# Optimization experiments

Measured on AMD Instinct MI355X. Metric: run time of the kernel, lower is better.

Reference implementation:

```python
import jax, jax.numpy as jnp
import numpy as np

# Malvar-He-Cutler demosaic kernels: 4 output feature maps from the 1-channel bayer mosaic.
_K = [
    0, 0, -2, 0, 0,  0, 0, 4, 0, 0,  -2, 4, 8, 4, -2,  0, 0, 4, 0, 0,  0, 0, -2, 0, 0,
    0, 0, -3, 0, 0,  0, 4, 0, 4, 0,  -3, 0, 12, 0, -3,  0, 4, 0, 4, 0,  0, 0, -3, 0, 0,
    0, 0, 1, 0, 0,  0, -2, 0, -2, 0,  -2, 8, 10, 8, -2,  0, -2, 0, -2, 0,  0, 0, 1, 0, 0,
    0, 0, -2, 0, 0,  0, -2, 8, -2, 0,  1, 0, 10, 0, 1,  0, -2, 8, -2, 0,  0, 0, -2, 0, 0,
]
KERNELS = jnp.asarray(np.asarray(_K, dtype=np.float32).reshape(4, 1, 5, 5) / 16.0)
# Per-output-channel (R,G,B), per-quadrant (2x2) source channel into feats=(conv4 || x) -> 5 channels.
INDICES_RGGB = np.array([4, 2, 3, 1, 0, 4, 4, 0, 1, 3, 2, 4]).reshape(1, 3, 2, 2)


def _calc_index(pattern):
    p = tuple(np.asarray(pattern).flatten().tolist())
    if p == (0, 1, 1, 2):
        return INDICES_RGGB
    if p == (1, 0, 2, 1):
        return np.roll(INDICES_RGGB, 1, axis=-1)
    if p == (1, 2, 0, 1):
        return np.roll(INDICES_RGGB, 1, axis=-2)
    if p == (2, 1, 1, 0):
        return np.roll(np.roll(INDICES_RGGB, 1, axis=-1), 1, axis=-2)
    raise ValueError('Invalid bayer pattern')


def _pixel_shuffle(x, r):
    N, C, H, W = x.shape
    c = C // (r * r)
    return x.reshape(N, c, r, r, H, W).transpose(0, 1, 4, 2, 5, 3).reshape(N, c, H * r, W * r)


def _gather_bayer(x, index):
    """x: (N, C_in, H, W); index: (1|N, C_out, 2, 2) -> (N, C_out, H, W).
    Efficient equivalent of the original one-hot mask multiply-sum: a direct
    per-quadrant channel selection via take_along_axis."""
    N, C, H, W = x.shape
    iN, Cout = index.shape[0], index.shape[1]
    h, w = H // 2, W // 2
    # pixel_unshuffle(x,2) with channel order c*4 + (2*i + j): quadrant axis q.
    xq = x.reshape(N, C, h, 2, w, 2).transpose(0, 1, 3, 5, 2, 4).reshape(N, C, 4, h, w)
    xq = xq.swapaxes(1, 2)  # (N, 4, C, h, w)
    iq = index.reshape(iN, Cout, 4).swapaxes(1, 2)  # (iN, 4, Cout)
    iq = jnp.broadcast_to(iq, (N, 4, Cout))
    gath = jnp.take_along_axis(xq, iq[:, :, :, None, None], axis=2)  # (N, 4, Cout, h, w)
    y_down = gath.swapaxes(1, 2).reshape(N, Cout * 4, h, w)
    return _pixel_shuffle(y_down, 2)


def setup_inputs() -> dict:
    key = jax.random.key(0)
    x = jax.random.uniform(key, (16, 1, 1024, 1024), dtype=jnp.float32)
    bayer_pattern = jnp.array([0, 1, 1, 2], dtype=jnp.int64 if jax.config.jax_enable_x64 else jnp.int32).reshape(1, 1, 2, 2)  # RGGB
    return {"x": x, "bayer_pattern": bayer_pattern}


def reference(x, bayer_pattern) -> jnp.ndarray:
    # Replication pad by 2 on each side, then 5x5 conv producing 4 feature maps.
    x_pad = jnp.pad(x, ((0, 0), (0, 0), (2, 2), (2, 2)), mode='edge')
    feats = jax.lax.conv_general_dilated(
        x_pad, KERNELS.astype(x.dtype), window_strides=(1, 1), padding='VALID',
        dimension_numbers=('NCHW', 'OIHW', 'NCHW'))
    feats = jnp.concatenate([feats, x], axis=1)  # (N, 5, H, W)
    bp = np.asarray(bayer_pattern)  # bayer pattern is static metadata
    index = jnp.asarray(np.concatenate([_calc_index(bp[n]) for n in range(bp.shape[0])], axis=0))
    return _gather_bayer(feats, index)  # (N, 3, H, W)
```

## Files before the change

kernel.cpp:

```cpp
#include <hip/hip_runtime.h>


constexpr int H = 1024, W = 1024;
constexpr int TILE_W = 128, TILE_H = 32;
constexpr int LDS_W = TILE_W + 4;
constexpr int LDS_H = TILE_H + 4;
constexpr int CHUNKS_PER_ROW = LDS_W / 4;
constexpr int N_CHUNKS = CHUNKS_PER_ROW * LDS_H;

typedef float v4f __attribute__((ext_vector_type(4)));
typedef __attribute__((address_space(1))) const unsigned int gu32;
typedef __attribute__((address_space(3))) unsigned int lu32;

__global__ __launch_bounds__(256) void demosaic_kernel(
    const float* __restrict__ xin_all, const int* __restrict__ bp,
    float* __restrict__ out)
{
    __shared__ float tile[LDS_H][LDS_W];

    const int tx = threadIdx.x;
    const int ty = threadIdx.y;
    const int tid = ty * 32 + tx;
    const int x0 = blockIdx.x * TILE_W;
    const int y0 = blockIdx.y * TILE_H;
    const int n  = blockIdx.z;

    const int p0 = bp[0], p1 = bp[1];
    const int fi = (p0 == 2) || (p0 == 1 && p1 == 2);
    const int fj = (p0 == 2) || (p0 == 1 && p1 == 0);

    const float* __restrict__ xin = xin_all + (size_t)n * H * W;

    const int gx0 = x0 - 2;
    for (int idx = tid; idx < N_CHUNKS; idx += 256) {
        const int r = idx / CHUNKS_PER_ROW;
        const int k = idx - r * CHUNKS_PER_ROW;
        const int gy = min(max(y0 + r - 2, 0), H - 1);
        const int gx = min(max(gx0 + 4 * k, 0), W - 4);
        const float* src = xin + (size_t)gy * W + gx;
        __builtin_amdgcn_global_load_lds((gu32*)src, (lu32*)&tile[r][4 * k], 16, 0, 0);
    }
    __syncthreads();

    const bool left_edge  = (x0 == 0);
    const bool right_edge = (x0 == W - TILE_W);
    if (left_edge || right_edge) {
        if (tid < LDS_H) {
            const int r  = tid;
            const int gy = min(max(y0 + r - 2, 0), H - 1);
            const float* __restrict__ rowp = xin + (size_t)gy * W;
            if (left_edge) {
                tile[r][0] = rowp[0]; tile[r][1] = rowp[0];
                tile[r][2] = rowp[0]; tile[r][3] = rowp[1];
            }
            if (right_edge) {
                tile[r][128] = rowp[W - 2]; tile[r][129] = rowp[W - 1];
                tile[r][130] = rowp[W - 1]; tile[r][131] = rowp[W - 1];
            }
        }
        __syncthreads();
    }

    const int xs  = tx * 4;
    const int ry0 = ty * 4;

    float w[8][8];
    #pragma unroll
    for (int r = 0; r < 8; ++r) {
        const v4f a = *(const v4f*)&tile[ry0 + r][xs];
        const v4f b = *(const v4f*)&tile[ry0 + r][xs + 4];
        w[r][0] = a.x; w[r][1] = a.y; w[r][2] = a.z; w[r][3] = a.w;
        w[r][4] = b.x; w[r][5] = b.y; w[r][6] = b.z; w[r][7] = b.w;
    }

    #pragma unroll
    for (int dr = 0; dr < 4; ++dr) {
        const int qi = (dr & 1) ^ fi;

        float r4[4], g4[4], b4[4];
        #pragma unroll
        for (int p = 0; p < 4; ++p) {
            const float c   = w[dr + 2][p + 2];
            const float up  = w[dr + 1][p + 2], dn  = w[dr + 3][p + 2];
            const float lf  = w[dr + 2][p + 1], rt  = w[dr + 2][p + 3];
            const float up2 = w[dr + 0][p + 2], dn2 = w[dr + 4][p + 2];
            const float lf2 = w[dr + 2][p + 0], rt2 = w[dr + 2][p + 4];
            const float dg  = w[dr + 1][p + 1] + w[dr + 1][p + 3]
                            + w[dr + 3][p + 1] + w[dr + 3][p + 3];

            const float axH = lf2 + rt2;
            const float axV = up2 + dn2;
            const float ax  = axH + axV;
            const float crossHV = (up + dn) + (lf + rt);

            const float s0 = (8.0f  * c + 4.0f * crossHV   - 2.0f * ax) * 0.0625f;
            const float s1 = (12.0f * c + 4.0f * dg        - 3.0f * ax) * 0.0625f;
            const float s2 = (10.0f * c + 8.0f * (lf + rt) - 2.0f * (axH + dg) + axV) * 0.0625f;
            const float s3 = (10.0f * c + 8.0f * (up + dn) - 2.0f * (axV + dg) + axH) * 0.0625f;

            const int qj = (p & 1) ^ fj;
            const int qt = (qi << 1) | qj;
            r4[p] = (qt == 0) ? c  : (qt == 1) ? s2 : (qt == 2) ? s3 : s1;
            g4[p] = (qi == qj) ? s0 : c;
            b4[p] = (qt == 0) ? s1 : (qt == 1) ? s3 : (qt == 2) ? s2 : c;
        }

        const int y = y0 + ry0 + dr;
        const size_t colbase = (size_t)(x0 + xs);
        v4f* __restrict__ oR = (v4f*)(out + ((size_t)(n * 3 + 0) * H + y) * W + colbase);
        v4f* __restrict__ oG = (v4f*)(out + ((size_t)(n * 3 + 1) * H + y) * W + colbase);
        v4f* __restrict__ oB = (v4f*)(out + ((size_t)(n * 3 + 2) * H + y) * W + colbase);
        v4f vR = { r4[0], r4[1], r4[2], r4[3] };
        v4f vG = { g4[0], g4[1], g4[2], g4[3] };
        v4f vB = { b4[0], b4[1], b4[2], b4[3] };
        __builtin_nontemporal_store(vR, oR);
        __builtin_nontemporal_store(vG, oG);
        __builtin_nontemporal_store(vB, oB);
    }
}

extern "C" void kernel_launch(void* const* d_in, const int* in_sizes, int n_in,
                              void* d_out, int out_size, void* d_ws, size_t ws_size,
                              hipStream_t stream) {
    const float* x  = (const float*)d_in[0];
    const int*   bp = (const int*)d_in[1];
    float* out = (float*)d_out;
    const int N = in_sizes[0] / (H * W);
    dim3 grid(W / TILE_W, H / TILE_H, N);
    dim3 block(32, 8, 1);
    demosaic_kernel<<<grid, block, 0, stream>>>(x, bp, out);
}
```

Baseline: 244.3 us.

## Double-buffer LDS tiles across four row-tiles per block with async prefetch

Each block now processes four vertical tiles, using two LDS buffers. The global→LDS load of the next tile is issued before the current tile is computed, with manual vmcnt waits and barriers. Edge replication moves from a separate LDS fixup pass into register fixups inside a new rolling 5-row register window, and launch bounds request higher occupancy. The goal is to hide load latency and cut per-block overhead. The risks are the hand-counted vmcnt values, since the stores also count toward vmcnt, and a smaller grid.

```diff
diff --git a/kernel.cpp b/kernel.cpp
--- a/kernel.cpp
+++ b/kernel.cpp
@@ -3,6 +3,7 @@
 
 constexpr int H = 1024, W = 1024;
 constexpr int TILE_W = 128, TILE_H = 32;
+constexpr int NT = 4;
 constexpr int LDS_W = TILE_W + 4;
 constexpr int LDS_H = TILE_H + 4;
 constexpr int CHUNKS_PER_ROW = LDS_W / 4;
@@ -12,17 +13,17 @@
 typedef __attribute__((address_space(1))) const unsigned int gu32;
 typedef __attribute__((address_space(3))) unsigned int lu32;
 
-__global__ __launch_bounds__(256) void demosaic_kernel(
+__global__ __launch_bounds__(256, 4) void demosaic_kernel(
     const float* __restrict__ xin_all, const int* __restrict__ bp,
     float* __restrict__ out)
 {
-    __shared__ float tile[LDS_H][LDS_W];
+    __shared__ float tile[2][LDS_H][LDS_W];
 
     const int tx = threadIdx.x;
     const int ty = threadIdx.y;
     const int tid = ty * 32 + tx;
     const int x0 = blockIdx.x * TILE_W;
-    const int y0 = blockIdx.y * TILE_H;
+    const int ybase = blockIdx.y * (TILE_H * NT);
     const int n  = blockIdx.z;
 
     const int p0 = bp[0], p1 = bp[1];
@@ -30,93 +31,125 @@
     const int fj = (p0 == 2) || (p0 == 1 && p1 == 0);
 
     const float* __restrict__ xin = xin_all + (size_t)n * H * W;
+    const int gx0 = x0 - 2;
 
-    const int gx0 = x0 - 2;
-    for (int idx = tid; idx < N_CHUNKS; idx += 256) {
-        const int r = idx / CHUNKS_PER_ROW;
-        const int k = idx - r * CHUNKS_PER_ROW;
-        const int gy = min(max(y0 + r - 2, 0), H - 1);
-        const int gx = min(max(gx0 + 4 * k, 0), W - 4);
-        const float* src = xin + (size_t)gy * W + gx;
-        __builtin_amdgcn_global_load_lds((gu32*)src, (lu32*)&tile[r][4 * k], 16, 0, 0);
+    int rr[5]  = {0, 0, 0, 0, 0};
+    int gxo[5] = {0, 0, 0, 0, 0};
+    #pragma unroll
+    for (int j = 0; j < 5; ++j) {
+        const int idx = tid + 256 * j;
+        if (idx < N_CHUNKS) {
+            const int r = idx / CHUNKS_PER_ROW;
+            const int k = idx - r * CHUNKS_PER_ROW;
+            rr[j]  = r;
+            gxo[j] = min(max(gx0 + 4 * k, 0), W - 4);
+        }
     }
-    __syncthreads();
 
-    const bool left_edge  = (x0 == 0);
-    const bool right_edge = (x0 == W - TILE_W);
-    if (left_edge || right_edge) {
-        if (tid < LDS_H) {
-            const int r  = tid;
-            const int gy = min(max(y0 + r - 2, 0), H - 1);
-            const float* __restrict__ rowp = xin + (size_t)gy * W;
-            if (left_edge) {
-                tile[r][0] = rowp[0]; tile[r][1] = rowp[0];
-                tile[r][2] = rowp[0]; tile[r][3] = rowp[1];
-            }
-            if (right_edge) {
-                tile[r][128] = rowp[W - 2]; tile[r][129] = rowp[W - 1];
-                tile[r][130] = rowp[W - 1]; tile[r][131] = rowp[W - 1];
+    auto STAGE = [&](int buf, int y0) {
+        float* const base = &tile[buf][0][0];
+        #pragma unroll
+        for (int j = 0; j < 5; ++j) {
+            const int idx = tid + 256 * j;
+            if (idx < N_CHUNKS) {
+                const int gy = min(max(y0 + rr[j] - 2, 0), H - 1);
+                __builtin_amdgcn_global_load_lds(
+                    (gu32*)(xin + (size_t)gy * W + gxo[j]),
+                    (lu32*)(base + 4 * idx), 16, 0, 0);
             }
         }
-        __syncthreads();
-    }
+    };
+
+    const bool lfix = (x0 == 0) && (tx == 0);
+    const bool rfix = (x0 == W - TILE_W) && (tx == 31);
 
     const int xs  = tx * 4;
     const int ry0 = ty * 4;
 
-    float w[8][8];
-    #pragma unroll
-    for (int r = 0; r < 8; ++r) {
-        const v4f a = *(const v4f*)&tile[ry0 + r][xs];
-        const v4f b = *(const v4f*)&tile[ry0 + r][xs + 4];
-        w[r][0] = a.x; w[r][1] = a.y; w[r][2] = a.z; w[r][3] = a.w;
-        w[r][4] = b.x; w[r][5] = b.y; w[r][6] = b.z; w[r][7] = b.w;
-    }
+    auto LOAD_ROW = [&](float (&d)[8], const float* p) {
+        const v4f a = *(const v4f*)p;
+        const v4f b = *(const v4f*)(p + 4);
+        d[0] = a.x; d[1] = a.y; d[2] = a.z; d[3] = a.w;
+        d[4] = b.x; d[5] = b.y; d[6] = b.z; d[7] = b.w;
+        if (lfix) { d[3] = d[1]; d[1] = d[0]; d[2] = d[0]; }
+        if (rfix) { d[4] = d[6]; d[5] = d[7]; d[6] = d[7]; }
+    };
 
-    #pragma unroll
-    for (int dr = 0; dr < 4; ++dr) {
-        const int qi = (dr & 1) ^ fi;
+    auto COMPUTE = [&](int buf, int y0) {
+        float w[5][8];
+        #pragma unroll
+        for (int m = 0; m < 4; ++m) LOAD_ROW(w[m], &tile[buf][ry0 + m][xs]);
 
-        float r4[4], g4[4], b4[4];
         #pragma unroll
-        for (int p = 0; p < 4; ++p) {
-            const float c   = w[dr + 2][p + 2];
-            const float up  = w[dr + 1][p + 2], dn  = w[dr + 3][p + 2];
-            const float lf  = w[dr + 2][p + 1], rt  = w[dr + 2][p + 3];
-            const float up2 = w[dr + 0][p + 2], dn2 = w[dr + 4][p + 2];
-            const float lf2 = w[dr + 2][p + 0], rt2 = w[dr + 2][p + 4];
-            const float dg  = w[dr + 1][p + 1] + w[dr + 1][p + 3]
-                            + w[dr + 3][p + 1] + w[dr + 3][p + 3];
+        for (int dr = 0; dr < 4; ++dr) {
+            LOAD_ROW(w[(dr + 4) % 5], &tile[buf][ry0 + dr + 4][xs]);
+            #define WR_(m) (w[(dr + (m)) % 5])
+            const int qi = (dr & 1) ^ fi;
 
-            const float axH = lf2 + rt2;
-            const float axV = up2 + dn2;
-            const float ax  = axH + axV;
-            const float crossHV = (up + dn) + (lf + rt);
+            float r4[4], g4[4], b4[4];
+            #pragma unroll
+            for (int p = 0; p < 4; ++p) {
+                const float c   = WR_(2)[p + 2];
+                const float up  = WR_(1)[p + 2], dn  = WR_(3)[p + 2];
+                const float lf  = WR_(2)[p + 1], rt  = WR_(2)[p + 3];
+                const float up2 = WR_(0)[p + 2], dn2 = WR_(4)[p + 2];
+                const float lf2 = WR_(2)[p + 0], rt2 = WR_(2)[p + 4];
+                const float dg  = WR_(1)[p + 1] + WR_(1)[p + 3]
+                                + WR_(3)[p + 1] + WR_(3)[p + 3];
 
-            const float s0 = (8.0f  * c + 4.0f * crossHV   - 2.0f * ax) * 0.0625f;
-            const float s1 = (12.0f * c + 4.0f * dg        - 3.0f * ax) * 0.0625f;
-            const float s2 = (10.0f * c + 8.0f * (lf + rt) - 2.0f * (axH + dg) + axV) * 0.0625f;
-            const float s3 = (10.0f * c + 8.0f * (up + dn) - 2.0f * (axV + dg) + axH) * 0.0625f;
+                const float axH = lf2 + rt2;
+                const float axV = up2 + dn2;
+                const float ax  = axH + axV;
+                const float crossHV = (up + dn) + (lf + rt);
 
-            const int qj = (p & 1) ^ fj;
-            const int qt = (qi << 1) | qj;
-            r4[p] = (qt == 0) ? c  : (qt == 1) ? s2 : (qt == 2) ? s3 : s1;
-            g4[p] = (qi == qj) ? s0 : c;
-            b4[p] = (qt == 0) ? s1 : (qt == 1) ? s3 : (qt == 2) ? s2 : c;
+                const float s0 = (8.0f  * c + 4.0f * crossHV   - 2.0f * ax) * 0.0625f;
+                const float s1 = (12.0f * c + 4.0f * dg        - 3.0f * ax) * 0.0625f;
+                const float s2 = (10.0f * c + 8.0f * (lf + rt) - 2.0f * (axH + dg) + axV) * 0.0625f;
+                const float s3 = (10.0f * c + 8.0f * (up + dn) - 2.0f * (axV + dg) + axH) * 0.0625f;
+
+                const int qj = (p & 1) ^ fj;
+                const int qt = (qi << 1) | qj;
+                r4[p] = (qt == 0) ? c  : (qt == 1) ? s2 : (qt == 2) ? s3 : s1;
+                g4[p] = (qi == qj) ? s0 : c;
+                b4[p] = (qt == 0) ? s1 : (qt == 1) ? s3 : (qt == 2) ? s2 : c;
+            }
+            #undef WR_
+
+            const int y = y0 + ry0 + dr;
+            const size_t colbase = (size_t)(x0 + xs);
+            v4f* const oR = (v4f*)(out + ((size_t)(n * 3 + 0) * H + y) * W + colbase);
+            v4f* const oG = (v4f*)(out + ((size_t)(n * 3 + 1) * H + y) * W + colbase);
+            v4f* const oB = (v4f*)(out + ((size_t)(n * 3 + 2) * H + y) * W + colbase);
+            v4f vR = { r4[0], r4[1], r4[2], r4[3] };
+            v4f vG = { g4[0], g4[1], g4[2], g4[3] };
+            v4f vB = { b4[0], b4[1], b4[2], b4[3] };
+            __builtin_nontemporal_store(vR, oR);
+            __builtin_nontemporal_store(vG, oG);
+            __builtin_nontemporal_store(vB, oB);
         }
+    };
 
-        const int y = y0 + ry0 + dr;
-        const size_t colbase = (size_t)(x0 + xs);
-        v4f* __restrict__ oR = (v4f*)(out + ((size_t)(n * 3 + 0) * H + y) * W + colbase);
-        v4f* __restrict__ oG = (v4f*)(out + ((size_t)(n * 3 + 1) * H + y) * W + colbase);
-        v4f* __restrict__ oB = (v4f*)(out + ((size_t)(n * 3 + 2) * H + y) * W + colbase);
-        v4f vR = { r4[0], r4[1], r4[2], r4[3] };
-        v4f vG = { g4[0], g4[1], g4[2], g4[3] };
-        v4f vB = { b4[0], b4[1], b4[2], b4[3] };
-        __builtin_nontemporal_store(vR, oR);
-        __builtin_nontemporal_store(vG, oG);
-        __builtin_nontemporal_store(vB, oB);
-    }
+    STAGE(0, ybase + 0 * TILE_H);
+    STAGE(1, ybase + 1 * TILE_H);
+    asm volatile("s_waitcnt vmcnt(4)" ::: "memory");
+    __builtin_amdgcn_s_barrier();
+    COMPUTE(0, ybase + 0 * TILE_H);
+    __builtin_amdgcn_s_barrier();
+
+    STAGE(0, ybase + 2 * TILE_H);
+    asm volatile("s_waitcnt vmcnt(16)" ::: "memory");
+    __builtin_amdgcn_s_barrier();
+    COMPUTE(1, ybase + 1 * TILE_H);
+    __builtin_amdgcn_s_barrier();
+
+    STAGE(1, ybase + 3 * TILE_H);
+    asm volatile("s_waitcnt vmcnt(16)" ::: "memory");
+    __builtin_amdgcn_s_barrier();
+    COMPUTE(0, ybase + 2 * TILE_H);
+
+    asm volatile("s_waitcnt vmcnt(12)" ::: "memory");
+    __builtin_amdgcn_s_barrier();
+    COMPUTE(1, ybase + 3 * TILE_H);
 }
 
 extern "C" void kernel_launch(void* const* d_in, const int* in_sizes, int n_in,
@@ -126,7 +159,7 @@
     const int*   bp = (const int*)d_in[1];
     float* out = (float*)d_out;
     const int N = in_sizes[0] / (H * W);
-    dim3 grid(W / TILE_W, H / TILE_H, N);
+    dim3 grid(W / TILE_W, H / (TILE_H * NT), N);
     dim3 block(32, 8, 1);
     demosaic_kernel<<<grid, block, 0, stream>>>(x, bp, out);
 }
```

After: 258.1 us. 1.06x slower.

## Replace LDS tiling with register sliding window over rows per thread

Applied to the files above, without the earlier changes.

Drops the shared-memory tile and barrier and has each thread walk 16 output rows. It keeps a 5-row rolling register window filled by direct vectorized global loads of the left, center and right 4-float chunks, and prefetches the next row while the current one is computed. Halo reuse now relies on L1/L2 rather than LDS, so each thread reloads neighbours' chunks three times per row. Block shape and tile size also change, and launch bounds ask for 4 blocks per CU.

```diff
diff --git a/kernel.cpp b/kernel.cpp
--- a/kernel.cpp
+++ b/kernel.cpp
@@ -2,28 +2,21 @@
 
 
 constexpr int H = 1024, W = 1024;
-constexpr int TILE_W = 128, TILE_H = 32;
-constexpr int LDS_W = TILE_W + 4;
-constexpr int LDS_H = TILE_H + 4;
-constexpr int CHUNKS_PER_ROW = LDS_W / 4;
-constexpr int N_CHUNKS = CHUNKS_PER_ROW * LDS_H;
+constexpr int TILE_W = 256, TILE_H = 64;
+constexpr int RPT = 16;
 
 typedef float v4f __attribute__((ext_vector_type(4)));
-typedef __attribute__((address_space(1))) const unsigned int gu32;
-typedef __attribute__((address_space(3))) unsigned int lu32;
 
-__global__ __launch_bounds__(256) void demosaic_kernel(
+__global__ __launch_bounds__(256, 4) void demosaic_kernel(
     const float* __restrict__ xin_all, const int* __restrict__ bp,
     float* __restrict__ out)
 {
-    __shared__ float tile[LDS_H][LDS_W];
-
     const int tx = threadIdx.x;
     const int ty = threadIdx.y;
-    const int tid = ty * 32 + tx;
     const int x0 = blockIdx.x * TILE_W;
-    const int y0 = blockIdx.y * TILE_H;
     const int n  = blockIdx.z;
+    const int gx = x0 + tx * 4;
+    const int ry0 = blockIdx.y * TILE_H + ty * RPT;
 
     const int p0 = bp[0], p1 = bp[1];
     const int fi = (p0 == 2) || (p0 == 1 && p1 == 2);
@@ -31,62 +24,54 @@
 
     const float* __restrict__ xin = xin_all + (size_t)n * H * W;
 
-    const int gx0 = x0 - 2;
-    for (int idx = tid; idx < N_CHUNKS; idx += 256) {
-        const int r = idx / CHUNKS_PER_ROW;
-        const int k = idx - r * CHUNKS_PER_ROW;
-        const int gy = min(max(y0 + r - 2, 0), H - 1);
-        const int gx = min(max(gx0 + 4 * k, 0), W - 4);
-        const float* src = xin + (size_t)gy * W + gx;
-        __builtin_amdgcn_global_load_lds((gu32*)src, (lu32*)&tile[r][4 * k], 16, 0, 0);
-    }
-    __syncthreads();
+    const bool lfix = (gx == 0);
+    const bool rfix = (gx == W - 4);
+    const int xl = lfix ? 0  : gx - 4;
+    const int xr = rfix ? gx : gx + 4;
 
-    const bool left_edge  = (x0 == 0);
-    const bool right_edge = (x0 == W - TILE_W);
-    if (left_edge || right_edge) {
-        if (tid < LDS_H) {
-            const int r  = tid;
-            const int gy = min(max(y0 + r - 2, 0), H - 1);
-            const float* __restrict__ rowp = xin + (size_t)gy * W;
-            if (left_edge) {
-                tile[r][0] = rowp[0]; tile[r][1] = rowp[0];
-                tile[r][2] = rowp[0]; tile[r][3] = rowp[1];
-            }
-            if (right_edge) {
-                tile[r][128] = rowp[W - 2]; tile[r][129] = rowp[W - 1];
-                tile[r][130] = rowp[W - 1]; tile[r][131] = rowp[W - 1];
-            }
-        }
-        __syncthreads();
-    }
+    float w[5][8];
 
-    const int xs  = tx * 4;
-    const int ry0 = ty * 4;
+    auto LOADROW = [&](int gy, v4f& L, v4f& M, v4f& R) {
+        gy = min(max(gy, 0), H - 1);
+        const float* row = xin + (size_t)gy * W;
+        L = *(const v4f*)(row + xl);
+        M = *(const v4f*)(row + gx);
+        R = *(const v4f*)(row + xr);
+    };
+    auto INSERT = [&](float (&d)[8], v4f L, v4f M, v4f R) {
+        d[0] = lfix ? M.x : L.z;
+        d[1] = lfix ? M.x : L.w;
+        d[2] = M.x; d[3] = M.y; d[4] = M.z; d[5] = M.w;
+        d[6] = rfix ? M.w : R.x;
+        d[7] = rfix ? M.w : R.y;
+    };
 
-    float w[8][8];
-    #pragma unroll
-    for (int r = 0; r < 8; ++r) {
-        const v4f a = *(const v4f*)&tile[ry0 + r][xs];
-        const v4f b = *(const v4f*)&tile[ry0 + r][xs + 4];
-        w[r][0] = a.x; w[r][1] = a.y; w[r][2] = a.z; w[r][3] = a.w;
-        w[r][4] = b.x; w[r][5] = b.y; w[r][6] = b.z; w[r][7] = b.w;
+    {
+        v4f L[5], M[5], R[5];
+        #pragma unroll
+        for (int m = 0; m < 5; ++m) LOADROW(ry0 - 2 + m, L[m], M[m], R[m]);
+        #pragma unroll
+        for (int m = 0; m < 5; ++m) INSERT(w[m], L[m], M[m], R[m]);
     }
 
     #pragma unroll
-    for (int dr = 0; dr < 4; ++dr) {
+    for (int dr = 0; dr < RPT; ++dr) {
+        v4f Lp, Mp, Rp;
+        if (dr < RPT - 1) LOADROW(ry0 + dr + 3, Lp, Mp, Rp);
+
+        #define WR_(m) (w[(dr + (m)) % 5])
         const int qi = (dr & 1) ^ fi;
 
         float r4[4], g4[4], b4[4];
         #pragma unroll
         for (int p = 0; p < 4; ++p) {
-            const float c   = w[dr + 2][p + 2];
-            const float up  = w[dr + 1][p + 2], dn  = w[dr + 3][p + 2];
-            const float lf  = w[dr + 2][p + 1], rt  = w[dr + 2][p + 3];
-            const float up2 = w[dr + 0][p + 2], dn2 = w[dr + 4][p + 2];
-            const float lf2 = w[dr + 2][p + 0], rt2 = w[dr + 2][p + 4];
-            const float dg  = w[dr + 1][p + 1] + w[dr + 1][p + 3]
-                            + w[dr + 3][p + 1] + w[dr + 3][p + 3];
+            const float c   = WR_(2)[p + 2];
+            const float up  = WR_(1)[p + 2], dn  = WR_(3)[p + 2];
+            const float lf  = WR_(2)[p + 1], rt  = WR_(2)[p + 3];
+            const float up2 = WR_(0)[p + 2], dn2 = WR_(4)[p + 2];
+            const float lf2 = WR_(2)[p + 0], rt2 = WR_(2)[p + 4];
+            const float dg  = WR_(1)[p + 1] + WR_(1)[p + 3]
+                            + WR_(3)[p + 1] + WR_(3)[p + 3];
 
             const float axH = lf2 + rt2;
             const float axV = up2 + dn2;
@@ -104,18 +89,21 @@
             g4[p] = (qi == qj) ? s0 : c;
             b4[p] = (qt == 0) ? s1 : (qt == 1) ? s3 : (qt == 2) ? s2 : c;
         }
+        #undef WR_
 
-        const int y = y0 + ry0 + dr;
-        const size_t colbase = (size_t)(x0 + xs);
-        v4f* __restrict__ oR = (v4f*)(out + ((size_t)(n * 3 + 0) * H + y) * W + colbase);
-        v4f* __restrict__ oG = (v4f*)(out + ((size_t)(n * 3 + 1) * H + y) * W + colbase);
-        v4f* __restrict__ oB = (v4f*)(out + ((size_t)(n * 3 + 2) * H + y) * W + colbase);
+        const int y = ry0 + dr;
+        const size_t rowoff = (size_t)y * W + gx;
+        v4f* const oR = (v4f*)(out + (size_t)(n * 3 + 0) * H * W + rowoff);
+        v4f* const oG = (v4f*)(out + (size_t)(n * 3 + 1) * H * W + rowoff);
+        v4f* const oB = (v4f*)(out + (size_t)(n * 3 + 2) * H * W + rowoff);
         v4f vR = { r4[0], r4[1], r4[2], r4[3] };
         v4f vG = { g4[0], g4[1], g4[2], g4[3] };
         v4f vB = { b4[0], b4[1], b4[2], b4[3] };
         __builtin_nontemporal_store(vR, oR);
         __builtin_nontemporal_store(vG, oG);
         __builtin_nontemporal_store(vB, oB);
+
+        if (dr < RPT - 1) INSERT(w[dr % 5], Lp, Mp, Rp);
     }
 }
 
@@ -127,6 +115,6 @@
     float* out = (float*)d_out;
     const int N = in_sizes[0] / (H * W);
     dim3 grid(W / TILE_W, H / TILE_H, N);
-    dim3 block(32, 8, 1);
+    dim3 block(64, 4, 1);
     demosaic_kernel<<<grid, block, 0, stream>>>(x, bp, out);
 }
```

Result: slower. 253.8 us (+3.9%).
